# Optimization experiments

Measured on AMD Instinct MI355X. Metric: run time of the kernel, lower is better.

The kernel has to match this reference:

```python
import jax, jax.numpy as jnp
import numpy as np

N = 100000
E = 1600000
IN_DIM = 128
HID = 128
C = 10
N_INJ = 20000
T_HET = 0.5          # self.hetero_level (set by set_adaptation_from_data)
HP_MAX = 1.0         # highpass_scale_max
INJ_LAM = 0.8        # self.inject_lambda


def setup_inputs() -> dict:
    key = jax.random.key(0)
    ks = jax.random.split(key, 16)
    glorot = lambda k, i, o: jax.random.normal(k, (i, o), jnp.float32) * (2.0 / (i + o)) ** 0.5
    return {
        "x": jax.random.normal(ks[0], (N, IN_DIM), jnp.float32),
        "edge_index": jax.random.randint(ks[1], (2, E), 0, N, jnp.int64),
        "inject_indices": jax.random.randint(ks[2], (N_INJ,), 0, N, jnp.int64),
        "initial_preds": jax.random.uniform(ks[3], (N, C), jnp.float32),
        "W1": glorot(ks[4], IN_DIM, HID), "b1": jnp.zeros((HID,), jnp.float32),
        "W2": glorot(ks[5], HID, HID),   "b2": jnp.zeros((HID,), jnp.float32),
        "Wl1": glorot(ks[6], IN_DIM, HID),
        "Wl2": glorot(ks[7], HID, HID),
        "Wm1": glorot(ks[8], HID, HID), "bm1": jnp.zeros((HID,), jnp.float32),
        "Wm2": glorot(ks[9], HID, C),   "bm2": jnp.zeros((C,), jnp.float32),
    }


def _gcn_norm(edge_index):
    # add self loops, symmetric D^{-1/2} (A+I) D^{-1/2} normalization (PyG GCNConv default)
    loops = jnp.arange(N, dtype=edge_index.dtype)
    src = jnp.concatenate([edge_index[0], loops])
    dst = jnp.concatenate([edge_index[1], loops])
    deg = jax.ops.segment_sum(jnp.ones_like(dst, jnp.float32), dst, num_segments=N)
    dinv = jnp.where(deg > 0, jax.lax.rsqrt(jnp.maximum(deg, 1.0)), 0.0)
    norm = dinv[src] * dinv[dst]  # [E+N]
    return src, dst, norm


def _gcn_conv(x, W, b, src, dst, norm):
    h = x @ W                                   # [N, H]
    msg = h[src] * norm[:, None]                # gather + scale, [E+N, H]
    return jax.ops.segment_sum(msg, dst, num_segments=N) + b


def reference(x, edge_index, inject_indices, initial_preds,
              W1, b1, W2, b2, Wl1, Wl2, Wm1, bm1, Wm2, bm2):
    src, dst, norm = _gcn_norm(edge_index)
    mix = T_HET * HP_MAX

    low1 = _gcn_conv(x, W1, b1, src, dst, norm)
    high1 = x @ Wl1 - low1
    h = jax.nn.relu(low1 + mix * high1)        # dropout: eval mode (identity)

    low2 = _gcn_conv(h, W2, b2, src, dst, norm)
    high2 = h @ Wl2 - low2
    h2 = low2 + mix * high2

    logits = jax.nn.relu(h2 @ Wm1 + bm1) @ Wm2 + bm2   # [N, C]
    # indexed injection: logits[idx] = logits[idx] + lam * preds[idx]
    logits = logits.at[inject_indices].set(
        logits[inject_indices] + INJ_LAM * initial_preds[inject_indices])
    return jax.nn.log_softmax(logits, axis=1)
```

## Files before the change

### kernel.cpp

```cpp
#include <hip/hip_runtime.h>
#include <hip/hip_bf16.h>
#include <math.h>

typedef __attribute__((ext_vector_type(8))) short short8;
typedef __attribute__((ext_vector_type(4))) float f32x4;

#define INJ_LAM 0.8f

__device__ inline float bf2f(unsigned short s){
  union{unsigned u; float f;} v; v.u=((unsigned)s)<<16; return v.f;
}
__device__ inline unsigned short f2bf(float f){
  __hip_bfloat16 h=__float2bfloat16(f);
  return *reinterpret_cast<unsigned short*>(&h);
}
__device__ inline unsigned pack2(float lo, float hi){
  return ((unsigned)f2bf(hi)<<16)|(unsigned)f2bf(lo);
}

__global__ void k_count_mark(const int* __restrict__ dst, unsigned* __restrict__ cnt,
                             unsigned* __restrict__ rank,
                             const int* __restrict__ inj, unsigned char* __restrict__ flag,
                             int E, int NI){
  int i=blockIdx.x*blockDim.x+threadIdx.x;
  if(i<E) rank[i]=atomicAdd(&cnt[dst[i]],1u);
  if(i<NI) flag[inj[i]]=1;
}

__global__ void k_scan_a(const unsigned* __restrict__ cnt, unsigned* __restrict__ bsum, int N){
  __shared__ unsigned sh[256];
  int t=threadIdx.x, b=blockIdx.x;
  int base=b*1024+t*4;
  unsigned ts=0;
  #pragma unroll
  for(int j=0;j<4;j++){ int i=base+j; if(i<N) ts+=cnt[i]; }
  sh[t]=ts; __syncthreads();
  for(int off=128;off>0;off>>=1){ if(t<off) sh[t]+=sh[t+off]; __syncthreads(); }
  if(t==0) bsum[b]=sh[0];
}

__global__ void k_scan_b(const unsigned* __restrict__ bsum, unsigned* __restrict__ bo, int NB){
  if(threadIdx.x==0 && blockIdx.x==0){
    unsigned run=0;
    for(int i=0;i<NB;i++){ bo[i]=run; run+=bsum[i]; }
  }
}

__global__ void k_scan_c(const unsigned* __restrict__ cnt, const unsigned* __restrict__ bo,
                         unsigned* __restrict__ offs,
                         float* __restrict__ dinv, int N){
  __shared__ unsigned sh[256];
  int t=threadIdx.x, b=blockIdx.x;
  int base=b*1024+t*4;
  unsigned c[4]; unsigned ts=0;
  #pragma unroll
  for(int j=0;j<4;j++){ int i=base+j; c[j]=(i<N)?cnt[i]:0u; ts+=c[j]; }
  sh[t]=ts; __syncthreads();
  for(int off=1;off<256;off<<=1){
    unsigned v=(t>=off)?sh[t-off]:0u; __syncthreads();
    sh[t]+=v; __syncthreads();
  }
  unsigned run=sh[t]-ts+bo[b];
  #pragma unroll
  for(int j=0;j<4;j++){
    int i=base+j;
    if(i<N){ offs[i]=run; dinv[i]=rsqrtf((float)(c[j]+1u)); }
    run+=c[j];
  }
}

__global__ void k_place(const int* __restrict__ src, const int* __restrict__ dst,
                        const unsigned* __restrict__ rank, const unsigned* __restrict__ offs,
                        int* __restrict__ csr, int E){
  int e=blockIdx.x*blockDim.x+threadIdx.x;
  if(e<E) csr[offs[dst[e]]+rank[e]]=src[e];
}

__global__ void k_prepw(const float* __restrict__ W1,const float* __restrict__ Wl1,
                        const float* __restrict__ W2,const float* __restrict__ Wl2,
                        const float* __restrict__ Wm1,const float* __restrict__ Wm2,
                        unsigned short* __restrict__ Wt1, unsigned short* __restrict__ Wt2,
                        unsigned short* __restrict__ Wm1t, unsigned short* __restrict__ Wm2tp){
  int i=blockIdx.x*blockDim.x+threadIdx.x;
  if(i<256*128){
    int c=i>>7, k=i&127;
    float v1=(c<128)?W1[k*128+c]:Wl1[k*128+(c-128)];
    float v2=(c<128)?W2[k*128+c]:Wl2[k*128+(c-128)];
    Wt1[i]=f2bf(v1); Wt2[i]=f2bf(v2);
    if(c<128) Wm1t[i]=f2bf(Wm1[k*128+c]);
    if(c<16)  Wm2tp[i]=f2bf((c<10)?Wm2[k*10+c]:0.f);
  }
}

template<bool FP32IN>
__device__ inline void load_afrag(const void* __restrict__ Xv, size_t arow, int l4, short8* a){
  if(FP32IN){
    const float* X=(const float*)Xv + arow*128 + l4*8;
    #pragma unroll
    for(int ks=0;ks<4;ks++){
      float4 f0=*reinterpret_cast<const float4*>(X+ks*32);
      float4 f1=*reinterpret_cast<const float4*>(X+ks*32+4);
      short8 t;
      t[0]=(short)f2bf(f0.x); t[1]=(short)f2bf(f0.y); t[2]=(short)f2bf(f0.z); t[3]=(short)f2bf(f0.w);
      t[4]=(short)f2bf(f1.x); t[5]=(short)f2bf(f1.y); t[6]=(short)f2bf(f1.z); t[7]=(short)f2bf(f1.w);
      a[ks]=t;
    }
  }else{
    const unsigned short* X=(const unsigned short*)Xv + arow*128 + l4*8;
    #pragma unroll
    for(int ks=0;ks<4;ks++)
      a[ks]=*reinterpret_cast<const short8*>(X+ks*32);
  }
}

template<bool FP32IN>
__launch_bounds__(256, 4)
__global__ void k_gemm(const void* __restrict__ Xv, const unsigned short* __restrict__ Wt,
                       const float* __restrict__ dinv,
                       unsigned short* __restrict__ G, unsigned short* __restrict__ XL, int N){
  int wave=threadIdx.x>>6, lane=threadIdx.x&63;
  int l15=lane&15, l4=lane>>4;
  int blk0=blockIdx.x*128;
  if(blk0>=N) return;
  short8 wf[4][4];
  #pragma unroll
  for(int i=0;i<4;i++){
    int col=(wave*4+i)*16+l15;
    #pragma unroll
    for(int ks=0;ks<4;ks++)
      wf[i][ks]=*reinterpret_cast<const short8*>(Wt+(size_t)col*128+ks*32+l4*8);
  }
  int r0=blk0+l15; if(r0>N-1) r0=N-1;
  short8 aC[4], aN[4];
  load_afrag<FP32IN>(Xv,(size_t)r0,l4,aC);
  #pragma unroll 1
  for(int nt=0;nt<8;nt++){
    int node0=blk0+nt*16;
    if(node0>=N) break;
    if(nt<7){
      int rn=node0+16+l15; if(rn>N-1) rn=N-1;
      load_afrag<FP32IN>(Xv,(size_t)rn,l4,aN);
    }
    f32x4 acc[4];
    #pragma unroll
    for(int i=0;i<4;i++) acc[i]=(f32x4){0.f,0.f,0.f,0.f};
    #pragma unroll
    for(int i=0;i<4;i++){
      #pragma unroll
      for(int ks=0;ks<4;ks++)
        acc[i]=__builtin_amdgcn_mfma_f32_16x16x32_bf16(wf[i][ks],aC[ks],acc[i],0,0,0);
    }
    int node=node0+l15;
    if(node<N){
      if(wave<2){
        float dv=dinv[node];
        #pragma unroll
        for(int i=0;i<4;i++){
          f32x4 v=acc[i];
          uint2 p; p.x=pack2(v[0]*dv,v[1]*dv); p.y=pack2(v[2]*dv,v[3]*dv);
          *reinterpret_cast<uint2*>(G+(size_t)node*128+(wave*4+i)*16+l4*4)=p;
        }
      }else{
        #pragma unroll
        for(int i=0;i<4;i++){
          f32x4 v=acc[i];
          uint2 p; p.x=pack2(v[0],v[1]); p.y=pack2(v[2],v[3]);
          *reinterpret_cast<uint2*>(XL+(size_t)node*128+((wave-2)*4+i)*16+l4*4)=p;
        }
      }
    }
    #pragma unroll
    for(int ks=0;ks<4;ks++) aC[ks]=aN[ks];
  }
}

#define ADDROW(acc,v) do{ \
  unsigned _x=(unsigned)(v).x,_y=(unsigned)(v).y,_z=(unsigned)(v).z,_w=(unsigned)(v).w; \
  acc[0]+=bf2f((unsigned short)(_x&0xffffu)); acc[1]+=bf2f((unsigned short)(_x>>16)); \
  acc[2]+=bf2f((unsigned short)(_y&0xffffu)); acc[3]+=bf2f((unsigned short)(_y>>16)); \
  acc[4]+=bf2f((unsigned short)(_z&0xffffu)); acc[5]+=bf2f((unsigned short)(_z>>16)); \
  acc[6]+=bf2f((unsigned short)(_w&0xffffu)); acc[7]+=bf2f((unsigned short)(_w>>16)); }while(0)

template<bool RELU>
__launch_bounds__(256)
__global__ void k_conv(const unsigned short* __restrict__ G, const unsigned short* __restrict__ XL,
                       const float* __restrict__ bias, const float* __restrict__ dinv,
                       const int* __restrict__ csr, const unsigned* __restrict__ offs,
                       const unsigned* __restrict__ cnt,
                       unsigned short* __restrict__ H, int N){
  int node=blockIdx.x*4+(threadIdx.x>>6);
  if(node>=N) return;
  int lane=threadIdx.x&63;
  int g=lane>>4, li=lane&15;
  const int4* Gv=(const int4*)G;
  float acc[8];
  #pragma unroll
  for(int i=0;i<8;i++) acc[i]=0.f;
  if(g==0){
    int4 v=Gv[(size_t)node*16+li];
    ADDROW(acc,v);
  }
  unsigned start=offs[node], deg=cnt[node];
  unsigned j=(unsigned)g;
  if(j<deg){
    int4 v=Gv[(size_t)csr[start+j]*16+li];
    j+=4;
    while(j<deg){
      int4 vn=Gv[(size_t)csr[start+j]*16+li];
      ADDROW(acc,v);
      v=vn; j+=4;
    }
    ADDROW(acc,v);
  }
  #pragma unroll
  for(int i=0;i<8;i++){
    acc[i]+=__shfl_xor(acc[i],16,64);
    acc[i]+=__shfl_xor(acc[i],32,64);
  }
  if(g==0){
    float dv=dinv[node];
    float4 b0=*reinterpret_cast<const float4*>(bias+li*8);
    float4 b1=*reinterpret_cast<const float4*>(bias+li*8+4);
    int4 xv=((const int4*)XL)[(size_t)node*16+li];
    float xl[8];
    { unsigned _x=(unsigned)xv.x,_y=(unsigned)xv.y,_z=(unsigned)xv.z,_w=(unsigned)xv.w;
      xl[0]=bf2f((unsigned short)(_x&0xffffu)); xl[1]=bf2f((unsigned short)(_x>>16));
      xl[2]=bf2f((unsigned short)(_y&0xffffu)); xl[3]=bf2f((unsigned short)(_y>>16));
      xl[4]=bf2f((unsigned short)(_z&0xffffu)); xl[5]=bf2f((unsigned short)(_z>>16));
      xl[6]=bf2f((unsigned short)(_w&0xffffu)); xl[7]=bf2f((unsigned short)(_w>>16)); }
    float bb[8]={b0.x,b0.y,b0.z,b0.w,b1.x,b1.y,b1.z,b1.w};
    float r[8];
    #pragma unroll
    for(int i=0;i<8;i++){
      r[i]=0.5f*(dv*acc[i]+bb[i])+0.5f*xl[i];
      if(RELU) r[i]=fmaxf(r[i],0.f);
    }
    int4 o;
    o.x=(int)pack2(r[0],r[1]); o.y=(int)pack2(r[2],r[3]);
    o.z=(int)pack2(r[4],r[5]); o.w=(int)pack2(r[6],r[7]);
    ((int4*)H)[(size_t)node*16+li]=o;
  }
}

__launch_bounds__(256)
__global__ void k_mlp(const unsigned short* __restrict__ H2,
                      const unsigned short* __restrict__ Wm1t,
                      const unsigned short* __restrict__ Wm2tp,
                      const float* __restrict__ bm1, const float* __restrict__ bm2,
                      const unsigned char* __restrict__ flag, const float* __restrict__ preds,
                      float* __restrict__ out, int N){
  __shared__ __align__(16) unsigned short zt[4][16][136];
  __shared__ __align__(16) float lt[4][16][16];
  int wave=threadIdx.x>>6, lane=threadIdx.x&63;
  int l15=lane&15, l4=lane>>4;
  int node0=blockIdx.x*64+wave*16;
  int arow=node0+l15; if(arow>N-1) arow=N-1; if(arow<0) arow=0;
  short8 a[4];
  #pragma unroll
  for(int ks=0;ks<4;ks++)
    a[ks]=*reinterpret_cast<const short8*>(H2+(size_t)arow*128+ks*32+l4*8);
  f32x4 acc[8];
  #pragma unroll
  for(int ct=0;ct<8;ct++) acc[ct]=(f32x4){0.f,0.f,0.f,0.f};
  #pragma unroll
  for(int ct=0;ct<8;ct++){
    #pragma unroll
    for(int ks=0;ks<4;ks++){
      short8 bfr=*reinterpret_cast<const short8*>(Wm1t+(size_t)(ct*16+l15)*128+ks*32+l4*8);
      acc[ct]=__builtin_amdgcn_mfma_f32_16x16x32_bf16(bfr,a[ks],acc[ct],0,0,0);
    }
  }
  #pragma unroll
  for(int ct=0;ct<8;ct++){
    float4 bm=*reinterpret_cast<const float4*>(bm1+ct*16+l4*4);
    uint2 p;
    p.x=pack2(fmaxf(acc[ct][0]+bm.x,0.f),fmaxf(acc[ct][1]+bm.y,0.f));
    p.y=pack2(fmaxf(acc[ct][2]+bm.z,0.f),fmaxf(acc[ct][3]+bm.w,0.f));
    *reinterpret_cast<uint2*>(&zt[wave][l15][ct*16+l4*4])=p;
  }
  __syncthreads();
  short8 a2[4];
  #pragma unroll
  for(int ks=0;ks<4;ks++)
    a2[ks]=*reinterpret_cast<const short8*>(&zt[wave][l15][ks*32+l4*8]);
  f32x4 acc2=(f32x4){0.f,0.f,0.f,0.f};
  #pragma unroll
  for(int ks=0;ks<4;ks++){
    short8 bfr=*reinterpret_cast<const short8*>(Wm2tp+(size_t)l15*128+ks*32+l4*8);
    acc2=__builtin_amdgcn_mfma_f32_16x16x32_bf16(bfr,a2[ks],acc2,0,0,0);
  }
  *reinterpret_cast<f32x4*>(&lt[wave][l15][l4*4])=acc2;
  __syncthreads();
  if(lane<16){
    int node=node0+lane;
    if(node<N){
      float v[10];
      #pragma unroll
      for(int c=0;c<10;c++) v[c]=lt[wave][lane][c]+bm2[c];
      if(flag[node]){
        #pragma unroll
        for(int c=0;c<10;c++) v[c]+=INJ_LAM*preds[(size_t)node*10+c];
      }
      float m=v[0];
      #pragma unroll
      for(int c=1;c<10;c++) m=fmaxf(m,v[c]);
      float s=0.f;
      #pragma unroll
      for(int c=0;c<10;c++) s+=expf(v[c]-m);
      float lse=m+logf(s);
      #pragma unroll
      for(int c=0;c<10;c++) out[(size_t)node*10+c]=v[c]-lse;
    }
  }
}

extern "C" void kernel_launch(void* const* d_in, const int* in_sizes, int n_in,
                              void* d_out, int out_size, void* d_ws, size_t ws_size,
                              hipStream_t stream){
  const float* x    =(const float*)d_in[0];
  const int*   ei   =(const int*)  d_in[1];
  const int*   inj  =(const int*)  d_in[2];
  const float* preds=(const float*)d_in[3];
  const float* W1 =(const float*)d_in[4];  const float* b1 =(const float*)d_in[5];
  const float* W2 =(const float*)d_in[6];  const float* b2 =(const float*)d_in[7];
  const float* Wl1=(const float*)d_in[8];  const float* Wl2=(const float*)d_in[9];
  const float* Wm1=(const float*)d_in[10]; const float* bm1=(const float*)d_in[11];
  const float* Wm2=(const float*)d_in[12]; const float* bm2=(const float*)d_in[13];
  float* out=(float*)d_out;

  const int N  = in_sizes[0]/128;
  const int E  = in_sizes[1]/2;
  const int NI = in_sizes[2];
  const int* srcp = ei;
  const int* dstp = ei+E;

  char* w=(char*)d_ws;
  auto carve=[&](size_t sz)->char*{ char* p=w; w+=(sz+255)&~(size_t)255; return p; };
  unsigned short* S0 =(unsigned short*)carve((size_t)N*128*2);
  unsigned short* S1 =(unsigned short*)carve((size_t)N*128*2);
  unsigned short* S2 =(unsigned short*)carve((size_t)N*128*2);
  unsigned short* Wt1=(unsigned short*)carve(256*128*2);
  unsigned short* Wt2=(unsigned short*)carve(256*128*2);
  unsigned short* Wm1t=(unsigned short*)carve(128*128*2);
  unsigned short* Wm2tp=(unsigned short*)carve(16*128*2);
  unsigned* cnt   =(unsigned*)carve((size_t)N*4);
  float*    dinv  =(float*)   carve((size_t)N*4);
  unsigned* offs  =(unsigned*)carve((size_t)N*4);
  unsigned* rank  =(unsigned*)carve((size_t)E*4);
  int*      csr   =(int*)     carve((size_t)E*4);
  unsigned char* flags=(unsigned char*)carve(((size_t)N+3)&~(size_t)3);
  const int NB=(N+1023)/1024;
  unsigned* bsum=(unsigned*)carve((size_t)NB*4);
  unsigned* bo  =(unsigned*)carve((size_t)NB*4);
  (void)ws_size; (void)n_in; (void)out_size;

  const int T=256;
  hipMemsetAsync(cnt, 0, (size_t)N*4, stream);
  hipMemsetAsync(flags, 0, (size_t)N, stream);
  hipLaunchKernelGGL(k_count_mark, dim3((E+T-1)/T), dim3(T), 0, stream, dstp, cnt, rank, inj, flags, E, NI);
  hipLaunchKernelGGL(k_scan_a, dim3(NB), dim3(T), 0, stream, cnt, bsum, N);
  hipLaunchKernelGGL(k_scan_b, dim3(1), dim3(64), 0, stream, bsum, bo, NB);
  hipLaunchKernelGGL(k_scan_c, dim3(NB), dim3(T), 0, stream, cnt, bo, offs, dinv, N);
  hipLaunchKernelGGL(k_place, dim3((E+T-1)/T), dim3(T), 0, stream, srcp, dstp, rank, offs, csr, E);
  hipLaunchKernelGGL(k_prepw, dim3(128), dim3(T), 0, stream, W1,Wl1,W2,Wl2,Wm1,Wm2, Wt1,Wt2,Wm1t,Wm2tp);

  dim3 gemmGrid((N+127)/128);
  hipLaunchKernelGGL(k_gemm<true>,  gemmGrid, dim3(T), 0, stream, (const void*)x,  Wt1, dinv, S1, S2, N);
  hipLaunchKernelGGL(k_conv<true>,  dim3((N+3)/4), dim3(T), 0, stream, S1, S2, b1, dinv, csr, offs, cnt, S0, N);
  hipLaunchKernelGGL(k_gemm<false>, gemmGrid, dim3(T), 0, stream, (const void*)S0, Wt2, dinv, S1, S2, N);
  hipLaunchKernelGGL(k_conv<false>, dim3((N+3)/4), dim3(T), 0, stream, S1, S2, b2, dinv, csr, offs, cnt, S0, N);
  hipLaunchKernelGGL(k_mlp, dim3((N+63)/64), dim3(T), 0, stream, S0, Wm1t, Wm2tp, bm1, bm2, flags, preds, out, N);
}
```

Before: 368.9 us.

## Build CSR via two-level bucket sort instead of global atomics and scan

```diff
diff --git a/kernel.cpp b/kernel.cpp
--- a/kernel.cpp
+++ b/kernel.cpp
@@ -6,6 +6,8 @@
 typedef __attribute__((ext_vector_type(4))) float f32x4;
 
 #define INJ_LAM 0.8f
+#define BSH 9
+#define BWD 512
 
 __device__ inline float bf2f(unsigned short s){
   union{unsigned u; float f;} v; v.u=((unsigned)s)<<16; return v.f;
@@ -18,62 +20,110 @@
   return ((unsigned)f2bf(hi)<<16)|(unsigned)f2bf(lo);
 }
 
-__global__ void k_count_mark(const int* __restrict__ dst, unsigned* __restrict__ cnt,
-                             unsigned* __restrict__ rank,
-                             const int* __restrict__ inj, unsigned char* __restrict__ flag,
-                             int E, int NI){
-  int i=blockIdx.x*blockDim.x+threadIdx.x;
-  if(i<E) rank[i]=atomicAdd(&cnt[dst[i]],1u);
+__global__ void k_bhist(const int* __restrict__ dst, unsigned* __restrict__ bhist8,
+                        const int* __restrict__ inj, unsigned char* __restrict__ flag,
+                        int E, int NI){
+  __shared__ unsigned lh[256];
+  int t=threadIdx.x;
+  lh[t]=0u;
+  int i=blockIdx.x*256+t;
   if(i<NI) flag[inj[i]]=1;
-}
-
-__global__ void k_scan_a(const unsigned* __restrict__ cnt, unsigned* __restrict__ bsum, int N){
-  __shared__ unsigned sh[256];
-  int t=threadIdx.x, b=blockIdx.x;
-  int base=b*1024+t*4;
-  unsigned ts=0;
-  #pragma unroll
-  for(int j=0;j<4;j++){ int i=base+j; if(i<N) ts+=cnt[i]; }
-  sh[t]=ts; __syncthreads();
-  for(int off=128;off>0;off>>=1){ if(t<off) sh[t]+=sh[t+off]; __syncthreads(); }
-  if(t==0) bsum[b]=sh[0];
-}
-
-__global__ void k_scan_b(const unsigned* __restrict__ bsum, unsigned* __restrict__ bo, int NB){
-  if(threadIdx.x==0 && blockIdx.x==0){
-    unsigned run=0;
-    for(int i=0;i<NB;i++){ bo[i]=run; run+=bsum[i]; }
-  }
-}
-
-__global__ void k_scan_c(const unsigned* __restrict__ cnt, const unsigned* __restrict__ bo,
-                         unsigned* __restrict__ offs,
-                         float* __restrict__ dinv, int N){
-  __shared__ unsigned sh[256];
-  int t=threadIdx.x, b=blockIdx.x;
-  int base=b*1024+t*4;
-  unsigned c[4]; unsigned ts=0;
-  #pragma unroll
-  for(int j=0;j<4;j++){ int i=base+j; c[j]=(i<N)?cnt[i]:0u; ts+=c[j]; }
-  sh[t]=ts; __syncthreads();
+  __syncthreads();
+  int base=blockIdx.x*2048;
+  #pragma unroll
+  for(int k=0;k<8;k++){
+    int e=base+k*256+t;
+    if(e<E) atomicAdd(&lh[dst[e]>>BSH],1u);
+  }
+  __syncthreads();
+  if(lh[t]) atomicAdd(&bhist8[t*8],lh[t]);
+}
+
+__global__ void k_bscan(const unsigned* __restrict__ bhist8, unsigned* __restrict__ bbase,
+                        unsigned* __restrict__ bcur8, int NBK){
+  __shared__ unsigned ss[256];
+  int t=threadIdx.x;
+  unsigned v=(t<NBK)?bhist8[t*8]:0u;
+  ss[t]=v; __syncthreads();
   for(int off=1;off<256;off<<=1){
-    unsigned v=(t>=off)?sh[t-off]:0u; __syncthreads();
-    sh[t]+=v; __syncthreads();
-  }
-  unsigned run=sh[t]-ts+bo[b];
-  #pragma unroll
-  for(int j=0;j<4;j++){
-    int i=base+j;
-    if(i<N){ offs[i]=run; dinv[i]=rsqrtf((float)(c[j]+1u)); }
-    run+=c[j];
-  }
-}
-
-__global__ void k_place(const int* __restrict__ src, const int* __restrict__ dst,
-                        const unsigned* __restrict__ rank, const unsigned* __restrict__ offs,
-                        int* __restrict__ csr, int E){
-  int e=blockIdx.x*blockDim.x+threadIdx.x;
-  if(e<E) csr[offs[dst[e]]+rank[e]]=src[e];
+    unsigned u=(t>=off)?ss[t-off]:0u; __syncthreads();
+    ss[t]+=u; __syncthreads();
+  }
+  unsigned excl=ss[t]-v;
+  if(t<NBK){ bbase[t]=excl; bcur8[t*8]=excl; }
+  if(t==255) bbase[NBK]=ss[255];
+}
+
+__global__ void k_bscatter(const int* __restrict__ src, const int* __restrict__ dst,
+                           unsigned* __restrict__ bcur8,
+                           int* __restrict__ psrc, int* __restrict__ pdst, int E){
+  __shared__ unsigned lh[256];
+  __shared__ unsigned gb[256];
+  int t=threadIdx.x;
+  lh[t]=0u; __syncthreads();
+  int base=blockIdx.x*2048;
+  unsigned lr[8]; int bk[8], sv[8], dv_[8];
+  #pragma unroll
+  for(int k=0;k<8;k++){
+    int e=base+k*256+t;
+    if(e<E){
+      int d=dst[e]; int b=d>>BSH;
+      bk[k]=b; dv_[k]=d; sv[k]=src[e];
+      lr[k]=atomicAdd(&lh[b],1u);
+    } else bk[k]=-1;
+  }
+  __syncthreads();
+  if(lh[t]) gb[t]=atomicAdd(&bcur8[t*8],lh[t]);
+  __syncthreads();
+  #pragma unroll
+  for(int k=0;k<8;k++){
+    if(bk[k]>=0){
+      unsigned p=gb[bk[k]]+lr[k];
+      psrc[p]=sv[k]; pdst[p]=dv_[k];
+    }
+  }
+}
+
+__launch_bounds__(256)
+__global__ void k_bucket(const int* __restrict__ psrc, const int* __restrict__ pdst,
+                         const unsigned* __restrict__ bbase, unsigned* __restrict__ rank,
+                         unsigned* __restrict__ cnt, unsigned* __restrict__ offs,
+                         float* __restrict__ dinv, int* __restrict__ csr, int N){
+  __shared__ unsigned lc[BWD];
+  __shared__ unsigned lo[BWD];
+  __shared__ unsigned ss[256];
+  int b=blockIdx.x, t=threadIdx.x;
+  unsigned e0=bbase[b], e1=bbase[b+1];
+  int lo_node=b<<BSH;
+  lc[t]=0u; lc[t+256]=0u; __syncthreads();
+  for(unsigned p=e0+t;p<e1;p+=256){
+    int dl=pdst[p]-lo_node;
+    rank[p]=atomicAdd(&lc[dl],1u);
+  }
+  __syncthreads();
+  unsigned c0=lc[2*t], c1=lc[2*t+1], ps=c0+c1;
+  ss[t]=ps; __syncthreads();
+  for(int off=1;off<256;off<<=1){
+    unsigned u=(t>=off)?ss[t-off]:0u; __syncthreads();
+    ss[t]+=u; __syncthreads();
+  }
+  unsigned excl=ss[t]-ps;
+  lo[2*t]=excl; lo[2*t+1]=excl+c0;
+  __syncthreads();
+  #pragma unroll
+  for(int k=0;k<2;k++){
+    int nl=t+k*256; int node=lo_node+nl;
+    if(node<N){
+      unsigned c=lc[nl];
+      cnt[node]=c;
+      offs[node]=e0+lo[nl];
+      dinv[node]=rsqrtf((float)(c+1u));
+    }
+  }
+  for(unsigned p=e0+t;p<e1;p+=256){
+    int dl=pdst[p]-lo_node;
+    csr[e0+lo[dl]+rank[p]]=psrc[p];
+  }
 }
 
 __global__ void k_prepw(const float* __restrict__ W1,const float* __restrict__ Wl1,
@@ -193,6 +243,7 @@
   int lane=threadIdx.x&63;
   int g=lane>>4, li=lane&15;
   const int4* Gv=(const int4*)G;
+  const int4 Z={0,0,0,0};
   float acc[8];
   #pragma unroll
   for(int i=0;i<8;i++) acc[i]=0.f;
@@ -202,16 +253,17 @@
   }
   unsigned start=offs[node], deg=cnt[node];
   unsigned j=(unsigned)g;
-  if(j<deg){
-    int4 v=Gv[(size_t)csr[start+j]*16+li];
-    j+=4;
-    while(j<deg){
-      int4 vn=Gv[(size_t)csr[start+j]*16+li];
-      ADDROW(acc,v);
-      v=vn; j+=4;
-    }
-    ADDROW(acc,v);
-  }
+  int4 v0=Z, v1=Z;
+  if(j<deg)   v0=Gv[(size_t)csr[start+j]*16+li];
+  if(j+4<deg) v1=Gv[(size_t)csr[start+j+4]*16+li];
+  j+=8;
+  while(j<deg){
+    int4 w0=Gv[(size_t)csr[start+j]*16+li];
+    int4 w1=(j+4<deg)?Gv[(size_t)csr[start+j+4]*16+li]:Z;
+    ADDROW(acc,v0); ADDROW(acc,v1);
+    v0=w0; v1=w1; j+=8;
+  }
+  ADDROW(acc,v0); ADDROW(acc,v1);
   #pragma unroll
   for(int i=0;i<8;i++){
     acc[i]+=__shfl_xor(acc[i],16,64);
@@ -333,6 +385,7 @@
   const int NI = in_sizes[2];
   const int* srcp = ei;
   const int* dstp = ei+E;
+  const int NBK = (N+BWD-1)>>BSH;
 
   char* w=(char*)d_ws;
   auto carve=[&](size_t sz)->char*{ char* p=w; w+=(sz+255)&~(size_t)255; return p; };
@@ -346,22 +399,26 @@
   unsigned* cnt   =(unsigned*)carve((size_t)N*4);
   float*    dinv  =(float*)   carve((size_t)N*4);
   unsigned* offs  =(unsigned*)carve((size_t)N*4);
-  unsigned* rank  =(unsigned*)carve((size_t)E*4);
   int*      csr   =(int*)     carve((size_t)E*4);
   unsigned char* flags=(unsigned char*)carve(((size_t)N+3)&~(size_t)3);
-  const int NB=(N+1023)/1024;
-  unsigned* bsum=(unsigned*)carve((size_t)NB*4);
-  unsigned* bo  =(unsigned*)carve((size_t)NB*4);
+  unsigned* bhist8=(unsigned*)carve(256*8*4);
+  unsigned* bcur8 =(unsigned*)carve(256*8*4);
+  unsigned* bbase =(unsigned*)carve(257*4);
   (void)ws_size; (void)n_in; (void)out_size;
 
+  int* psrc=(int*)S1;
+  int* pdst=psrc+E;
+  unsigned* rank=(unsigned*)S2;
+
   const int T=256;
-  hipMemsetAsync(cnt, 0, (size_t)N*4, stream);
+  const int EB=(E+2047)/2048;
+  hipMemsetAsync(bhist8, 0, 256*8*4, stream);
   hipMemsetAsync(flags, 0, (size_t)N, stream);
-  hipLaunchKernelGGL(k_count_mark, dim3((E+T-1)/T), dim3(T), 0, stream, dstp, cnt, rank, inj, flags, E, NI);
-  hipLaunchKernelGGL(k_scan_a, dim3(NB), dim3(T), 0, stream, cnt, bsum, N);
-  hipLaunchKernelGGL(k_scan_b, dim3(1), dim3(64), 0, stream, bsum, bo, NB);
-  hipLaunchKernelGGL(k_scan_c, dim3(NB), dim3(T), 0, stream, cnt, bo, offs, dinv, N);
-  hipLaunchKernelGGL(k_place, dim3((E+T-1)/T), dim3(T), 0, stream, srcp, dstp, rank, offs, csr, E);
+  hipLaunchKernelGGL(k_bhist, dim3(EB), dim3(T), 0, stream, dstp, bhist8, inj, flags, E, NI);
+  hipLaunchKernelGGL(k_bscan, dim3(1), dim3(T), 0, stream, bhist8, bbase, bcur8, NBK);
+  hipLaunchKernelGGL(k_bscatter, dim3(EB), dim3(T), 0, stream, srcp, dstp, bcur8, psrc, pdst, E);
+  hipLaunchKernelGGL(k_bucket, dim3(NBK), dim3(T), 0, stream, psrc, pdst, bbase, rank,
+                     cnt, offs, dinv, csr, N);
   hipLaunchKernelGGL(k_prepw, dim3(128), dim3(T), 0, stream, W1,Wl1,W2,Wl2,Wm1,Wm2, Wt1,Wt2,Wm1t,Wm2tp);
 
   dim3 gemmGrid((N+127)/128);
```

Result: faster. 353.9 us (-4.1%).
